# Performance work log

Hardware: AMD Instinct MI355X
Metric: run time of the kernel (lower is better)

Reference implementation:

```python
import jax, jax.numpy as jnp
import numpy as np

NBIT = 4          # weight bit-width
GROUP_SIZE = 128  # weight quantization group size (divides k)
HAS_WEIGHT_ZEROS = True


def _quant_dequant_weights(w, group_size=GROUP_SIZE, nbit=NBIT, has_zeros=HAS_WEIGHT_ZEROS):
    # Mirrors torchao _quantize + quantize_per_channel_group, then dequantizes
    # (the native kernel dequantizes inline with the matmul; math is identical).
    qmin = -(1 << (nbit - 1))
    qmax = (1 << (nbit - 1)) - 1
    n, k = w.shape
    g = w.reshape(-1, group_size)                      # [n*k/gs, gs]
    vmin = g.min(axis=1, keepdims=True)
    vmax = g.max(axis=1, keepdims=True)
    scales = (vmax - vmin) / (qmax - qmin)             # per-group scale
    if has_zeros:
        zeros = qmin - jnp.round(vmin / scales)
    else:
        zeros = jnp.zeros_like(scales)
    q = jnp.clip(jnp.round(g / scales) + zeros, qmin, qmax)
    deq = (q - zeros) * scales
    return deq.reshape(n, k)


def _dyn_quant_dequant_act(x):
    # Dynamic per-token (per-row) asymmetric int8 activation quantization.
    qmin, qmax = -128, 127
    xmin = x.min(axis=-1, keepdims=True)
    xmax = x.max(axis=-1, keepdims=True)
    scale = (xmax - xmin) / (qmax - qmin)
    zero = qmin - jnp.round(xmin / scale)
    q = jnp.clip(jnp.round(x / scale) + zero, qmin, qmax)
    return (q - zero) * scale


def setup_inputs() -> dict:
    key = jax.random.key(0)
    k1, k2 = jax.random.split(key)
    x = jax.random.normal(k1, (4, 2048, 4096), dtype=jnp.float32)
    weights = jax.random.normal(k2, (4096, 4096), dtype=jnp.float32) * 0.02
    return {"x": x, "weights": weights}


def reference(x, weights):
    w_deq = _quant_dequant_weights(weights)            # [n, k]
    x_deq = _dyn_quant_dequant_act(x)                  # [..., m, k]
    # y[..., m, n] = x_deq @ w_deq^T
    return jnp.einsum('bmk,nk->bmn', x_deq, w_deq)
```

## Files before the change

kernel.cpp:

```cpp
#include <hip/hip_runtime.h>
#include <hip/hip_bf16.h>
#include <cfloat>

typedef __attribute__((ext_vector_type(8))) short bf16x8;
typedef __attribute__((ext_vector_type(4))) float f32x4;

#define M_DIM 8192
#define N_DIM 4096
#define K_DIM 4096

__device__ inline ushort f2bf(float f) {
    unsigned u = __float_as_uint(f);
    unsigned r = (u + 0x7FFFu + ((u >> 16) & 1u)) >> 16;
    return (ushort)r;
}

#define SWZ(x) ((x) ^ ((((x) >> 7) & 7) << 4))

__global__ __launch_bounds__(256) void w_dq_pack(const float* __restrict__ w,
                                                 ushort* __restrict__ wq) {
    int bx = blockIdx.x;
    int n0 = (bx >> 5) * 64;
    int kg = bx & 31;
    int t = threadIdx.x;
    int n = n0 + (t >> 2);
    int kq = t & 3;
    const float* src = w + (size_t)n * K_DIM + kg * 128 + kq * 32;
    float4 v[8];
    float mn = FLT_MAX, mx = -FLT_MAX;
#pragma unroll
    for (int j = 0; j < 8; j++) {
        v[j] = ((const float4*)src)[j];
        mn = fminf(mn, fminf(fminf(v[j].x, v[j].y), fminf(v[j].z, v[j].w)));
        mx = fmaxf(mx, fmaxf(fmaxf(v[j].x, v[j].y), fmaxf(v[j].z, v[j].w)));
    }
    mn = fminf(mn, __shfl_xor(mn, 1)); mx = fmaxf(mx, __shfl_xor(mx, 1));
    mn = fminf(mn, __shfl_xor(mn, 2)); mx = fmaxf(mx, __shfl_xor(mx, 2));
    float scale = (mx - mn) / 15.0f;
    float zero  = -8.0f - rintf(mn / scale);

    int nb = n >> 8, wn = (n >> 6) & 3, ni = (n >> 4) & 3, lr = n & 15;
    int T = kg * 2 + (kq >> 1), kk = kq & 1;
    size_t base16 = ((((size_t)(nb * 4 + wn) * 64 + T) * 2 + kk) * 4 + ni) * 64;
#pragma unroll
    for (int lh = 0; lh < 4; lh++) {
        bf16x8 o;
#pragma unroll
        for (int e = 0; e < 8; e++) {
            float4 vv = v[lh * 2 + (e >> 2)];
            float x = (e & 3) == 0 ? vv.x : (e & 3) == 1 ? vv.y : (e & 3) == 2 ? vv.z : vv.w;
            float q = fminf(fmaxf(rintf(x / scale) + zero, -8.0f), 7.0f);
            o[e] = (short)f2bf((q - zero) * scale);
        }
        *(bf16x8*)(wq + (base16 + lh * 16 + lr) * 8) = o;
    }
}

__global__ __launch_bounds__(256) void act_qdq(const float* __restrict__ x,
                                               ushort* __restrict__ xq) {
    __shared__ float smn[4], smx[4];
    int row = blockIdx.x;
    const float* xr = x + (size_t)row * K_DIM;
    ushort* xo = xq + (size_t)row * K_DIM;
    int t = threadIdx.x;
    float4 v[4];
    float mn = FLT_MAX, mx = -FLT_MAX;
#pragma unroll
    for (int i = 0; i < 4; i++) {
        v[i] = ((const float4*)xr)[t + i * 256];
        mn = fminf(mn, fminf(fminf(v[i].x, v[i].y), fminf(v[i].z, v[i].w)));
        mx = fmaxf(mx, fmaxf(fmaxf(v[i].x, v[i].y), fmaxf(v[i].z, v[i].w)));
    }
#pragma unroll
    for (int s = 1; s < 64; s <<= 1) {
        mn = fminf(mn, __shfl_xor(mn, s));
        mx = fmaxf(mx, __shfl_xor(mx, s));
    }
    int w = t >> 6;
    if ((t & 63) == 0) { smn[w] = mn; smx[w] = mx; }
    __syncthreads();
    mn = fminf(fminf(smn[0], smn[1]), fminf(smn[2], smn[3]));
    mx = fmaxf(fmaxf(smx[0], smx[1]), fmaxf(smx[2], smx[3]));
    float scale = (mx - mn) / 255.0f;
    float zero  = -128.0f - rintf(mn / scale);
#pragma unroll
    for (int i = 0; i < 4; i++) {
        ushort4 o;
        float q;
        q = fminf(fmaxf(rintf(v[i].x / scale) + zero, -128.0f), 127.0f); o.x = f2bf((q - zero) * scale);
        q = fminf(fmaxf(rintf(v[i].y / scale) + zero, -128.0f), 127.0f); o.y = f2bf((q - zero) * scale);
        q = fminf(fmaxf(rintf(v[i].z / scale) + zero, -128.0f), 127.0f); o.z = f2bf((q - zero) * scale);
        q = fminf(fmaxf(rintf(v[i].w / scale) + zero, -128.0f), 127.0f); o.w = f2bf((q - zero) * scale);
        ((ushort4*)xo)[t + i * 256] = o;
    }
}

#define BM 256
#define BN 256
#define BK 64
#define NT (K_DIM / BK)

__global__ __launch_bounds__(512, 1) void gemm_bt8(const ushort* __restrict__ A,
                                                   const ushort* __restrict__ Bp,
                                                   float* __restrict__ C) {
    __shared__ __align__(16) ushort As[2][BM * BK];

    int orig = blockIdx.x;
    int xcd = orig & 7, j = orig >> 3;
    int nb = xcd * 2 + (j >> 5);
    int mb = j & 31;
    size_t m0 = (size_t)mb * BM;

    const int t = threadIdx.x;
    const int w = t >> 6, lane = t & 63;
    const int wm = w >> 2, wn = w & 3;
    const int lr = lane & 15;
    const int lk = (lane >> 4) << 3;

    const ushort* Ab = A + m0 * K_DIM;
    const ushort* Bpk = Bp + (size_t)(nb * 4 + wn) * 64 * 4096;

    f32x4 acc[8][4] = {};
    bf16x8 afr[4][2];
    bf16x8 bfr[4][2];

#define STAGEALL(dd, T) do {                                                      \
    _Pragma("unroll") for (int rq = 0; rq < 4; rq++) {                            \
        int base = rq * 8192 + w * 1024;                                          \
        int lb = base + lane * 16;                                                \
        int lg = SWZ(lb);                                                         \
        __builtin_amdgcn_global_load_lds(                                         \
            (const __attribute__((address_space(1))) unsigned int*)(Ab + (size_t)(lg >> 7) * K_DIM + (T) * BK + ((lg & 127) >> 1)), \
            (__attribute__((address_space(3))) unsigned int*)((char*)As[dd] + base), \
            16, 0, 0);                                                            \
    } } while (0)

#define LOADA_H(h, dd) do {                                                       \
    _Pragma("unroll") for (int mf = 0; mf < 4; mf++)                              \
    _Pragma("unroll") for (int kk = 0; kk < 2; kk++) {                            \
        int mi = (h) * 4 + mf;                                                    \
        int row = (mi >> 1) * 64 + wm * 32 + (mi & 1) * 16 + lr;                  \
        int lg = row * 128 + (kk * 32 + lk) * 2;                                  \
        afr[mf][kk] = *(const bf16x8*)((const char*)As[dd] + SWZ(lg));            \
    } } while (0)

#define LOADBG(T) do {                                                            \
    const ushort* bp = Bpk + (size_t)(T) * 4096;                                  \
    _Pragma("unroll") for (int kk = 0; kk < 2; kk++)                              \
    _Pragma("unroll") for (int ni = 0; ni < 4; ni++)                              \
        bfr[ni][kk] = *(const bf16x8*)(bp + ((kk * 4 + ni) * 64 + lane) * 8);     \
    } while (0)

#define MFMAH(h) do {                                                             \
    __builtin_amdgcn_s_setprio(1);                                                \
    _Pragma("unroll") for (int kk = 0; kk < 2; kk++)                              \
    _Pragma("unroll") for (int mf = 0; mf < 4; mf++)                              \
    _Pragma("unroll") for (int ni = 0; ni < 4; ni++)                              \
        acc[(h) * 4 + mf][ni] = __builtin_amdgcn_mfma_f32_16x16x32_bf16(          \
            afr[mf][kk], bfr[ni][kk], acc[(h) * 4 + mf][ni], 0, 0, 0);            \
    __builtin_amdgcn_s_setprio(0);                                                \
  } while (0)

#define ITER(d, T) do {                                                           \
    LOADBG(T);                                            \
    if ((T) + 1 < NT) STAGEALL((d) ^ 1, (T) + 1);                                 \
    LOADA_H(0, d);                                                                \
    asm volatile("s_waitcnt lgkmcnt(0)" ::: "memory");                            \
    __builtin_amdgcn_sched_barrier(0);                                            \
    MFMAH(0);                            \
    LOADA_H(1, d);                                                                \
    asm volatile("s_waitcnt lgkmcnt(0)" ::: "memory");                            \
    __builtin_amdgcn_sched_barrier(0);                                            \
    MFMAH(1);                                                                     \
    asm volatile("s_waitcnt vmcnt(0)" ::: "memory");      \
    __builtin_amdgcn_s_barrier();                                                 \
    __builtin_amdgcn_sched_barrier(0);                                            \
  } while (0)

    STAGEALL(0, 0);
    asm volatile("s_waitcnt vmcnt(0)" ::: "memory");
    __builtin_amdgcn_s_barrier();
    __builtin_amdgcn_sched_barrier(0);

#pragma unroll 1
    for (int i = 0; i < NT / 2; i++) {
        ITER(0, 2 * i);
        ITER(1, 2 * i + 1);
    }
#undef ITER
#undef MFMAH
#undef LOADBG
#undef LOADA_H
#undef STAGEALL

    size_t n0 = (size_t)nb * BN;
    int fq = lane >> 4;
#pragma unroll
    for (int mi = 0; mi < 8; mi++) {
#pragma unroll
        for (int ni = 0; ni < 4; ni++) {
#pragma unroll
            for (int r = 0; r < 4; r++) {
                size_t crow = m0 + (mi >> 1) * 64 + wm * 32 + (mi & 1) * 16 + fq * 4 + r;
                C[crow * N_DIM + n0 + wn * 64 + ni * 16 + lr] = acc[mi][ni][r];
            }
        }
    }
}

extern "C" void kernel_launch(void* const* d_in, const int* in_sizes, int n_in,
                              void* d_out, int out_size, void* d_ws, size_t ws_size,
                              hipStream_t stream) {
    const float* x = (const float*)d_in[0];
    const float* w = (const float*)d_in[1];
    float* out = (float*)d_out;

    ushort* wq = (ushort*)d_ws;
    ushort* xq = (ushort*)((char*)d_ws + (size_t)N_DIM * K_DIM * 2);

    hipLaunchKernelGGL(w_dq_pack, dim3((N_DIM / 64) * (K_DIM / 128)), dim3(256), 0, stream, w, wq);
    hipLaunchKernelGGL(act_qdq, dim3(M_DIM), dim3(256), 0, stream, x, xq);
    hipLaunchKernelGGL(gemm_bt8, dim3((M_DIM / BM) * (N_DIM / BN)), dim3(512), 0, stream, xq, wq, out);
}
```

Measured before the change: 354.9 us.

## Remap GEMM warp tiling to 4x2 layout with 64x128 per-warp tiles

Changes the per-warp tile from 128x64 (2 row-warps by 4 col-warps) to 64x128 (4 by 2), so each warp loads 8 B fragments directly from global memory per K-step and reads A from LDS in four small phases. This halves the LDS A-fragment traffic per warp and doubles the per-warp global B loads, and it interleaves each A load with its MFMA block at finer granularity. It relies on the packed B layout matching the new indexing and raises register pressure for the B fragments.

```diff
diff --git a/kernel.cpp b/kernel.cpp
--- a/kernel.cpp
+++ b/kernel.cpp
@@ -113,16 +113,16 @@
 
     const int t = threadIdx.x;
     const int w = t >> 6, lane = t & 63;
-    const int wm = w >> 2, wn = w & 3;
+    const int wm = w >> 1, wn = w & 1;
     const int lr = lane & 15;
     const int lk = (lane >> 4) << 3;
 
     const ushort* Ab = A + m0 * K_DIM;
-    const ushort* Bpk = Bp + (size_t)(nb * 4 + wn) * 64 * 4096;
-
-    f32x4 acc[8][4] = {};
-    bf16x8 afr[4][2];
-    bf16x8 bfr[4][2];
+    const int nbase = nb * 4 + wn * 2;
+
+    f32x4 acc[4][8] = {};
+    bf16x8 afr[2];
+    bf16x8 bfr[8][2];
 
 #define STAGEALL(dd, T) do {                                                      \
     _Pragma("unroll") for (int rq = 0; rq < 4; rq++) {                            \
@@ -135,43 +135,43 @@
             16, 0, 0);                                                            \
     } } while (0)
 
-#define LOADA_H(h, dd) do {                                                       \
-    _Pragma("unroll") for (int mf = 0; mf < 4; mf++)                              \
+#define LOADB_ALL(T) do {                                                         \
+    _Pragma("unroll") for (int ni = 0; ni < 8; ni++)                              \
+    _Pragma("unroll") for (int kk = 0; kk < 2; kk++)                              \
+        bfr[ni][kk] = *(const bf16x8*)(Bp +                                       \
+            ((((size_t)(nbase + (ni >> 2)) * 64 + (T)) * 2 + kk) * 4 + (ni & 3)) * 512 + lane * 8); \
+    } while (0)
+
+#define LOADA_PH(mi, dd) do {                                                     \
     _Pragma("unroll") for (int kk = 0; kk < 2; kk++) {                            \
-        int mi = (h) * 4 + mf;                                                    \
-        int row = (mi >> 1) * 64 + wm * 32 + (mi & 1) * 16 + lr;                  \
+        int row = wm * 64 + (mi) * 16 + lr;                                       \
         int lg = row * 128 + (kk * 32 + lk) * 2;                                  \
-        afr[mf][kk] = *(const bf16x8*)((const char*)As[dd] + SWZ(lg));            \
+        afr[kk] = *(const bf16x8*)((const char*)As[dd] + SWZ(lg));                \
     } } while (0)
 
-#define LOADBG(T) do {                                                            \
-    const ushort* bp = Bpk + (size_t)(T) * 4096;                                  \
-    _Pragma("unroll") for (int kk = 0; kk < 2; kk++)                              \
-    _Pragma("unroll") for (int ni = 0; ni < 4; ni++)                              \
-        bfr[ni][kk] = *(const bf16x8*)(bp + ((kk * 4 + ni) * 64 + lane) * 8);     \
-    } while (0)
-
-#define MFMAH(h) do {                                                             \
+#define MFMA_PH(mi) do {                                                          \
     __builtin_amdgcn_s_setprio(1);                                                \
     _Pragma("unroll") for (int kk = 0; kk < 2; kk++)                              \
-    _Pragma("unroll") for (int mf = 0; mf < 4; mf++)                              \
-    _Pragma("unroll") for (int ni = 0; ni < 4; ni++)                              \
-        acc[(h) * 4 + mf][ni] = __builtin_amdgcn_mfma_f32_16x16x32_bf16(          \
-            afr[mf][kk], bfr[ni][kk], acc[(h) * 4 + mf][ni], 0, 0, 0);            \
+    _Pragma("unroll") for (int ni = 0; ni < 8; ni++)                              \
+        acc[mi][ni] = __builtin_amdgcn_mfma_f32_16x16x32_bf16(                    \
+            afr[kk], bfr[ni][kk], acc[mi][ni], 0, 0, 0);                          \
     __builtin_amdgcn_s_setprio(0);                                                \
   } while (0)
 
-#define ITER(d, T) do {                                                           \
-    LOADBG(T);                                            \
-    if ((T) + 1 < NT) STAGEALL((d) ^ 1, (T) + 1);                                 \
-    LOADA_H(0, d);                                                                \
+#define PH(mi, dd) do {                                                           \
+    LOADA_PH(mi, dd);                                                             \
     asm volatile("s_waitcnt lgkmcnt(0)" ::: "memory");                            \
     __builtin_amdgcn_sched_barrier(0);                                            \
-    MFMAH(0);                            \
-    LOADA_H(1, d);                                                                \
-    asm volatile("s_waitcnt lgkmcnt(0)" ::: "memory");                            \
-    __builtin_amdgcn_sched_barrier(0);                                            \
-    MFMAH(1);                                                                     \
+    MFMA_PH(mi);                                                                  \
+  } while (0)
+
+#define ITER(d, T) do {                                                           \
+    LOADB_ALL(T);                                   \
+    if ((T) + 1 < NT) STAGEALL((d) ^ 1, (T) + 1);                                 \
+    PH(0, d);                              \
+    PH(1, d);                                                                     \
+    PH(2, d);                                                                     \
+    PH(3, d);                                                                     \
     asm volatile("s_waitcnt vmcnt(0)" ::: "memory");      \
     __builtin_amdgcn_s_barrier();                                                 \
     __builtin_amdgcn_sched_barrier(0);                                            \
@@ -188,21 +188,22 @@
         ITER(1, 2 * i + 1);
     }
 #undef ITER
-#undef MFMAH
-#undef LOADBG
-#undef LOADA_H
+#undef PH
+#undef MFMA_PH
+#undef LOADA_PH
+#undef LOADB_ALL
 #undef STAGEALL
 
     size_t n0 = (size_t)nb * BN;
     int fq = lane >> 4;
 #pragma unroll
-    for (int mi = 0; mi < 8; mi++) {
-#pragma unroll
-        for (int ni = 0; ni < 4; ni++) {
+    for (int mi = 0; mi < 4; mi++) {
+#pragma unroll
+        for (int ni = 0; ni < 8; ni++) {
 #pragma unroll
             for (int r = 0; r < 4; r++) {
-                size_t crow = m0 + (mi >> 1) * 64 + wm * 32 + (mi & 1) * 16 + fq * 4 + r;
-                C[crow * N_DIM + n0 + wn * 64 + ni * 16 + lr] = acc[mi][ni][r];
+                size_t crow = m0 + wm * 64 + mi * 16 + fq * 4 + r;
+                C[crow * N_DIM + n0 + wn * 128 + ni * 16 + lr] = acc[mi][ni][r];
             }
         }
     }
```

Measured after the change: 374.8 us. 5.6% more time.
